# Kernel optimization log

Hardware: AMD Instinct MI355X
Metric: run time of the kernel (lower is better)

The kernel has to match this reference:

```python
import jax, jax.numpy as jnp
import numpy as np

B, N, D = 8, 2048, 768

def setup_inputs() -> dict:
    key = jax.random.key(0)
    k1, k2, k3 = jax.random.split(key, 3)
    H = jax.random.normal(k1, (B, N, D), dtype=jnp.float32)
    doc_sents_h = jax.random.normal(k2, (B, N, D), dtype=jnp.float32)
    # nn.Linear(2D, 1): weight [1, 2D], bias [1]
    W_strengh = jax.random.normal(k3, (1, 2 * D), dtype=jnp.float32) * (1.0 / np.sqrt(2 * D))
    b_strengh = jnp.zeros((1,), dtype=jnp.float32)
    return {"H": H, "doc_sents_h": doc_sents_h, "W_strengh": W_strengh, "b_strengh": b_strengh}

def _edge_scores(x, W, b):
    # Linear(cat(x_src, x_dst)) = x_src @ Wa + x_dst @ Wb + b, avoiding the
    # huge [B,N,N,2D] concat the original materializes (same math).
    d = x.shape[-1]
    wa = W[0, :d]   # [D] applied to src half
    wb = W[0, d:]   # [D] applied to dst half
    s_src = jnp.einsum('bnd,d->bn', x, wa)  # [B,N]
    s_dst = jnp.einsum('bnd,d->bn', x, wb)  # [B,N]
    # pair (i,j): src index i (unsqueeze(-2) expand), dst index j (unsqueeze(-3))
    return jax.nn.relu(s_src[:, :, None] + s_dst[:, None, :] + b[0])  # [B,N,N]

def reference(H, doc_sents_h, W_strengh, b_strengh):
    pred_results = _edge_scores(H, W_strengh, b_strengh)
    doc_sents_h_pred_results = _edge_scores(doc_sents_h, W_strengh, b_strengh)
    return (pred_results, doc_sents_h_pred_results)
```

## Files before the change

kernel.cpp:

```cpp
#include <hip/hip_runtime.h>

#define BB 8
#define NN 2048
#define DD 768
#define BN (BB * NN)
#define ROWS (2 * BN)
#define RPB 16

typedef float f4 __attribute__((ext_vector_type(4)));

__global__ __launch_bounds__(256) void scores_kernel(
        const float* __restrict__ H,
        const float* __restrict__ Dh,
        const float* __restrict__ W,
        const float* __restrict__ bias,
        float* __restrict__ ssrc,
        float* __restrict__ sdst) {
    const int wave = threadIdx.x >> 6;
    const int lane = threadIdx.x & 63;
    const int row  = blockIdx.x * 4 + wave;

    const float* x = (row < BN) ? (H + (size_t)row * DD)
                                : (Dh + (size_t)(row - BN) * DD);
    const f4* x4  = reinterpret_cast<const f4*>(x);
    const f4* wa4 = reinterpret_cast<const f4*>(W);
    const f4* wb4 = reinterpret_cast<const f4*>(W + DD);

    float sa = 0.0f, sb = 0.0f;
#pragma unroll
    for (int w = 0; w < 3; ++w) {
        const int idx = lane + w * 64;
        const f4 xv = __builtin_nontemporal_load(&x4[idx]);
        const f4 av = wa4[idx];
        const f4 bv = wb4[idx];
        sa += xv.x * av.x + xv.y * av.y + xv.z * av.z + xv.w * av.w;
        sb += xv.x * bv.x + xv.y * bv.y + xv.z * bv.z + xv.w * bv.w;
    }
#pragma unroll
    for (int off = 32; off > 0; off >>= 1) {
        sa += __shfl_down(sa, off, 64);
        sb += __shfl_down(sb, off, 64);
    }
    if (lane == 0) {
        ssrc[row] = sa + bias[0];
        sdst[row] = sb;
    }
}

__global__ __launch_bounds__(256) void edges_kernel(
        const float* __restrict__ ssrc,
        const float* __restrict__ sdst,
        float* __restrict__ out) {
    const int row0  = blockIdx.x * RPB;
    const int group = (row0 / NN) * NN;
    const f4* sd4 = reinterpret_cast<const f4*>(sdst + group);
    const f4 d0 = sd4[threadIdx.x];
    const f4 d1 = sd4[threadIdx.x + 256];

    float s[RPB];
#pragma unroll
    for (int r = 0; r < RPB; ++r) s[r] = ssrc[row0 + r];

    f4* o4 = reinterpret_cast<f4*>(out + (size_t)row0 * NN);
#pragma unroll
    for (int r = 0; r < RPB; ++r) {
        f4 a, b;
        a.x = fmaxf(s[r] + d0.x, 0.0f);
        a.y = fmaxf(s[r] + d0.y, 0.0f);
        a.z = fmaxf(s[r] + d0.z, 0.0f);
        a.w = fmaxf(s[r] + d0.w, 0.0f);
        b.x = fmaxf(s[r] + d1.x, 0.0f);
        b.y = fmaxf(s[r] + d1.y, 0.0f);
        b.z = fmaxf(s[r] + d1.z, 0.0f);
        b.w = fmaxf(s[r] + d1.w, 0.0f);
        __builtin_nontemporal_store(a, &o4[(size_t)r * 512 + threadIdx.x]);
        __builtin_nontemporal_store(b, &o4[(size_t)r * 512 + threadIdx.x + 256]);
    }
}

extern "C" void kernel_launch(void* const* d_in, const int* in_sizes, int n_in,
                              void* d_out, int out_size, void* d_ws, size_t ws_size,
                              hipStream_t stream) {
    const float* H    = (const float*)d_in[0];
    const float* Dh   = (const float*)d_in[1];
    const float* W    = (const float*)d_in[2];
    const float* bias = (const float*)d_in[3];
    float* out  = (float*)d_out;

    float* ssrc = (float*)d_ws;
    float* sdst = ssrc + ROWS;

    scores_kernel<<<ROWS / 4, 256, 0, stream>>>(H, Dh, W, bias, ssrc, sdst);
    edges_kernel<<<ROWS / RPB, 256, 0, stream>>>(ssrc, sdst, out);
}
```

Before: 71.18 us.

## Cache weights in registers and process 16 rows per wave in score kernel

The score kernel now has each 16-lane subgroup compute a full row dot product, and each wave handles 16 rows across four iterations. Each lane keeps its slice of both weight vectors in registers, so W is loaded once instead of once per row, and the reduction needs only a 16-lane shuffle. The grid shrinks 16x, raising per-thread register use. The edge kernel also switches its output writes from nontemporal stores to plain stores, which changes the cache policy on the large output write.

```diff
diff --git a/kernel.cpp b/kernel.cpp
--- a/kernel.cpp
+++ b/kernel.cpp
@@ -18,32 +18,42 @@
         float* __restrict__ sdst) {
     const int wave = threadIdx.x >> 6;
     const int lane = threadIdx.x & 63;
-    const int row  = blockIdx.x * 4 + wave;
+    const int sub  = lane >> 4;
+    const int l16  = lane & 15;
 
-    const float* x = (row < BN) ? (H + (size_t)row * DD)
-                                : (Dh + (size_t)(row - BN) * DD);
-    const f4* x4  = reinterpret_cast<const f4*>(x);
     const f4* wa4 = reinterpret_cast<const f4*>(W);
     const f4* wb4 = reinterpret_cast<const f4*>(W + DD);
+    f4 wa[12], wb[12];
+#pragma unroll
+    for (int w = 0; w < 12; ++w) {
+        wa[w] = wa4[l16 + 16 * w];
+        wb[w] = wb4[l16 + 16 * w];
+    }
+    const float bb = bias[0];
 
-    float sa = 0.0f, sb = 0.0f;
+    const int row_base = (blockIdx.x * 4 + wave) * 16;
 #pragma unroll
-    for (int w = 0; w < 3; ++w) {
-        const int idx = lane + w * 64;
-        const f4 xv = __builtin_nontemporal_load(&x4[idx]);
-        const f4 av = wa4[idx];
-        const f4 bv = wb4[idx];
-        sa += xv.x * av.x + xv.y * av.y + xv.z * av.z + xv.w * av.w;
-        sb += xv.x * bv.x + xv.y * bv.y + xv.z * bv.z + xv.w * bv.w;
-    }
+    for (int q = 0; q < 4; ++q) {
+        const int row = row_base + q * 4 + sub;
+        const float* x = (row < BN) ? (H + (size_t)row * DD)
+                                    : (Dh + (size_t)(row - BN) * DD);
+        const f4* x4 = reinterpret_cast<const f4*>(x);
+        float sa = 0.0f, sb = 0.0f;
 #pragma unroll
-    for (int off = 32; off > 0; off >>= 1) {
-        sa += __shfl_down(sa, off, 64);
-        sb += __shfl_down(sb, off, 64);
-    }
-    if (lane == 0) {
-        ssrc[row] = sa + bias[0];
-        sdst[row] = sb;
+        for (int w = 0; w < 12; ++w) {
+            const f4 xv = x4[l16 + 16 * w];
+            sa += xv.x * wa[w].x + xv.y * wa[w].y + xv.z * wa[w].z + xv.w * wa[w].w;
+            sb += xv.x * wb[w].x + xv.y * wb[w].y + xv.z * wb[w].z + xv.w * wb[w].w;
+        }
+#pragma unroll
+        for (int off = 8; off > 0; off >>= 1) {
+            sa += __shfl_down(sa, off, 16);
+            sb += __shfl_down(sb, off, 16);
+        }
+        if (l16 == 0) {
+            ssrc[row] = sa + bb;
+            sdst[row] = sb;
+        }
     }
 }
 
@@ -73,8 +83,8 @@
         b.y = fmaxf(s[r] + d1.y, 0.0f);
         b.z = fmaxf(s[r] + d1.z, 0.0f);
         b.w = fmaxf(s[r] + d1.w, 0.0f);
-        __builtin_nontemporal_store(a, &o4[(size_t)r * 512 + threadIdx.x]);
-        __builtin_nontemporal_store(b, &o4[(size_t)r * 512 + threadIdx.x + 256]);
+        o4[(size_t)r * 512 + threadIdx.x]       = a;
+        o4[(size_t)r * 512 + threadIdx.x + 256] = b;
     }
 }
 
@@ -90,6 +100,6 @@
     float* ssrc = (float*)d_ws;
     float* sdst = ssrc + ROWS;
 
-    scores_kernel<<<ROWS / 4, 256, 0, stream>>>(H, Dh, W, bias, ssrc, sdst);
+    scores_kernel<<<ROWS / 64, 256, 0, stream>>>(H, Dh, W, bias, ssrc, sdst);
     edges_kernel<<<ROWS / RPB, 256, 0, stream>>>(ssrc, sdst, out);
 }
```

Result: slower. 83.50 us (+17.3%).

## Fuse score and edge kernels into one cooperative kernel with grid sync

Applied to the files above, without the earlier changes.

Replaces the two-kernel sequence with a single cooperative launch of 1024 persistent blocks. Each block first computes 32 row scores with the weights held in registers, then does a grid-wide sync, then writes its 32 output rows. The aim is to remove the second launch and the gap between kernels and to reuse the weight loads across rows. The cost is a grid barrier, and all 1024 blocks must be co-resident, so it relies on at least 4 blocks per CU. If the cooperative launch fails, the code falls back to the old two-kernel path.

```diff
diff --git a/kernel.cpp b/kernel.cpp
--- a/kernel.cpp
+++ b/kernel.cpp
@@ -1,13 +1,88 @@
 #include <hip/hip_runtime.h>
+#include <hip/hip_cooperative_groups.h>
+
+namespace cg = cooperative_groups;
 
 #define BB 8
 #define NN 2048
 #define DD 768
 #define BN (BB * NN)
 #define ROWS (2 * BN)
-#define RPB 16
+#define GRID 1024
+#define RPB (ROWS / GRID)
 
 typedef float f4 __attribute__((ext_vector_type(4)));
+
+__global__ __launch_bounds__(256, 4) void fused_kernel(
+        const float* __restrict__ H,
+        const float* __restrict__ Dh,
+        const float* __restrict__ W,
+        const float* __restrict__ bias,
+        float* __restrict__ ssrc,
+        float* __restrict__ sdst,
+        float* __restrict__ out) {
+    const int wave = threadIdx.x >> 6;
+    const int lane = threadIdx.x & 63;
+
+    const f4* wa4 = reinterpret_cast<const f4*>(W);
+    const f4* wb4 = reinterpret_cast<const f4*>(W + DD);
+    f4 wa[3], wb[3];
+#pragma unroll
+    for (int w = 0; w < 3; ++w) {
+        wa[w] = wa4[lane + w * 64];
+        wb[w] = wb4[lane + w * 64];
+    }
+    const float bb = bias[0];
+
+#pragma unroll
+    for (int i = 0; i < 8; ++i) {
+        const int row = blockIdx.x * RPB + wave * 8 + i;
+        const float* x = (row < BN) ? (H + (size_t)row * DD)
+                                    : (Dh + (size_t)(row - BN) * DD);
+        const f4* x4 = reinterpret_cast<const f4*>(x);
+        float sa = 0.0f, sb = 0.0f;
+#pragma unroll
+        for (int w = 0; w < 3; ++w) {
+            const f4 xv = __builtin_nontemporal_load(&x4[lane + w * 64]);
+            sa += xv.x * wa[w].x + xv.y * wa[w].y + xv.z * wa[w].z + xv.w * wa[w].w;
+            sb += xv.x * wb[w].x + xv.y * wb[w].y + xv.z * wb[w].z + xv.w * wb[w].w;
+        }
+#pragma unroll
+        for (int off = 32; off > 0; off >>= 1) {
+            sa += __shfl_down(sa, off, 64);
+            sb += __shfl_down(sb, off, 64);
+        }
+        if (lane == 0) {
+            ssrc[row] = sa + bb;
+            sdst[row] = sb;
+        }
+    }
+
+    cg::this_grid().sync();
+
+    const int row0  = blockIdx.x * RPB;
+    const int group = (row0 / NN) * NN;
+    const f4* sd4 = reinterpret_cast<const f4*>(sdst + group);
+    const f4 d0 = sd4[threadIdx.x];
+    const f4 d1 = sd4[threadIdx.x + 256];
+
+    f4* o4 = reinterpret_cast<f4*>(out + (size_t)row0 * NN);
+#pragma unroll
+    for (int r = 0; r < RPB; ++r) {
+        const float s = ssrc[row0 + r];
+        f4 a, b;
+        a.x = fmaxf(s + d0.x, 0.0f);
+        a.y = fmaxf(s + d0.y, 0.0f);
+        a.z = fmaxf(s + d0.z, 0.0f);
+        a.w = fmaxf(s + d0.w, 0.0f);
+        b.x = fmaxf(s + d1.x, 0.0f);
+        b.y = fmaxf(s + d1.y, 0.0f);
+        b.z = fmaxf(s + d1.z, 0.0f);
+        b.w = fmaxf(s + d1.w, 0.0f);
+        __builtin_nontemporal_store(a, &o4[(size_t)r * 512 + threadIdx.x]);
+        __builtin_nontemporal_store(b, &o4[(size_t)r * 512 + threadIdx.x + 256]);
+    }
+}
 
 __global__ __launch_bounds__(256) void scores_kernel(
         const float* __restrict__ H,
@@ -51,19 +126,19 @@
         const float* __restrict__ ssrc,
         const float* __restrict__ sdst,
         float* __restrict__ out) {
-    const int row0  = blockIdx.x * RPB;
+    const int row0  = blockIdx.x * 16;
     const int group = (row0 / NN) * NN;
     const f4* sd4 = reinterpret_cast<const f4*>(sdst + group);
     const f4 d0 = sd4[threadIdx.x];
     const f4 d1 = sd4[threadIdx.x + 256];
 
-    float s[RPB];
+    float s[16];
 #pragma unroll
-    for (int r = 0; r < RPB; ++r) s[r] = ssrc[row0 + r];
+    for (int r = 0; r < 16; ++r) s[r] = ssrc[row0 + r];
 
     f4* o4 = reinterpret_cast<f4*>(out + (size_t)row0 * NN);
 #pragma unroll
-    for (int r = 0; r < RPB; ++r) {
+    for (int r = 0; r < 16; ++r) {
         f4 a, b;
         a.x = fmaxf(s[r] + d0.x, 0.0f);
         a.y = fmaxf(s[r] + d0.y, 0.0f);
@@ -90,6 +165,13 @@
     float* ssrc = (float*)d_ws;
     float* sdst = ssrc + ROWS;
 
-    scores_kernel<<<ROWS / 4, 256, 0, stream>>>(H, Dh, W, bias, ssrc, sdst);
-    edges_kernel<<<ROWS / RPB, 256, 0, stream>>>(ssrc, sdst, out);
+    void* args[] = { (void*)&H, (void*)&Dh, (void*)&W, (void*)&bias,
+                     (void*)&ssrc, (void*)&sdst, (void*)&out };
+    hipError_t err = hipLaunchCooperativeKernel(
+        reinterpret_cast<void*>(fused_kernel), dim3(GRID), dim3(256),
+        args, 0, stream);
+    if (err != hipSuccess) {
+        scores_kernel<<<ROWS / 4, 256, 0, stream>>>(H, Dh, W, bias, ssrc, sdst);
+        edges_kernel<<<ROWS / 16, 256, 0, stream>>>(ssrc, sdst, out);
+    }
 }
```

After: 161.9 us. 2.28x slower.
